# Kernel optimization log

Measured on AMD Instinct MI355X. Metric: run time of the kernel, lower is better.

Reference implementation:

```python
import jax, jax.numpy as jnp
import numpy as np
import math

HEADS = 16
LAYER, NUM_LAYERS = 6, 12
ALPHA = 1.0 - math.tanh(math.pi * LAYER / NUM_LAYERS)
EPS = 1e-5


def _rot_half(t):
    d = t.shape[-1] // 2
    return jnp.concatenate([-t[..., d:], t[..., :d]], axis=-1)


def axial_rope(t):
    # t: [b, n, H, W, d]. Axial rotary: height rotates first d/2, width rotates second d/2.
    H, W, d = t.shape[2], t.shape[3], t.shape[4]
    half = d // 2
    inv_freq = 1.0 / (10000.0 ** (jnp.arange(0, half, 2, dtype=jnp.float32) / half))  # [half/2]
    ang_h = jnp.arange(H, dtype=jnp.float32)[:, None] * inv_freq[None, :]  # [H, half/2]
    ang_w = jnp.arange(W, dtype=jnp.float32)[:, None] * inv_freq[None, :]  # [W, half/2]
    ang_h = jnp.concatenate([ang_h, ang_h], axis=-1)  # [H, half]
    ang_w = jnp.concatenate([ang_w, ang_w], axis=-1)  # [W, half]
    ch, sh = jnp.cos(ang_h)[:, None, :], jnp.sin(ang_h)[:, None, :]  # [H,1,half]
    cw, sw = jnp.cos(ang_w)[None, :, :], jnp.sin(ang_w)[None, :, :]  # [1,W,half]
    th, tw = t[..., :half], t[..., half:]
    th = th * ch + _rot_half(th) * sh
    tw = tw * cw + _rot_half(tw) * sw
    return jnp.concatenate([th, tw], axis=-1)


def setup_inputs() -> dict:
    key = jax.random.key(0)
    ks = jax.random.split(key, 4)
    b, H, W, hid = 32, 28, 28, 1024
    return {
        "x": jax.random.normal(ks[0], (b, H, W, hid), jnp.float32),
        "input_img": jax.random.normal(ks[1], (b, H, W, hid), jnp.float32),
        "qkv_w": jax.random.normal(ks[2], (hid, 3 * hid), jnp.float32) * 0.02,
        "o_w": jax.random.normal(ks[3], (hid, hid), jnp.float32) * 0.02,
        "gn_w": jnp.ones((HEADS,), jnp.float32),
        "gn_b": jnp.zeros((HEADS,), jnp.float32),
    }


def reference(x, input_img, qkv_w, o_w, gn_w, gn_b):
    b, H, W, hid = x.shape
    n, dh = HEADS, hid // HEADS
    qkv = x @ qkv_w  # [b,H,W,3*hid]
    # 'b h w (c d) -> c b h w d'
    qkv = qkv.reshape(b, H, W, 3, hid).transpose(3, 0, 1, 2, 4)
    qkv = qkv + input_img[None] * ALPHA
    # 'c b h w (n d) -> c b n h w d'; unpack order is q, v, k
    qkv = qkv.reshape(3, b, H, W, n, dh).transpose(0, 1, 4, 2, 3, 5)
    q, v, k = qkv[0], qkv[1], qkv[2]
    gamma = (1.0 - 2.0 ** (-5.0 - jnp.arange(n, dtype=jnp.float32)))[None, :, None, None, None]
    k = k * gamma
    q, k = axial_rope(q), axial_rope(k)
    # attention along the W axis per row: [b,n,H,W,W]
    scores = jnp.einsum('bnhxd,bnhzd->bnhxz', q, k)
    # original einsum sums v over heights h as well as over y
    vsum = v.sum(axis=2)  # [b,n,W,dh]
    out = jnp.einsum('bnxwy,bnyd->bnxwd', scores, vsum)  # [b,n,H,W,dh]
    # GroupNorm(num_heads, num_heads): normalize each head over (H,W,dh)
    mu = out.mean(axis=(2, 3, 4), keepdims=True)
    var = out.var(axis=(2, 3, 4), keepdims=True)
    out = (out - mu) / jnp.sqrt(var + EPS)
    out = out * gn_w[None, :, None, None, None] + gn_b[None, :, None, None, None]
    # 'b n h w d -> b h w (n d)'
    out = out.transpose(0, 2, 3, 1, 4).reshape(b, H, W, hid)
    return out @ o_w
```

## Files before the change

kernel.cpp:

```cpp
#include <hip/hip_runtime.h>
#include <cstdint>
#include <cstddef>

#define HEADS 16
#define DH 64
#define BH 28
#define BWW 28
#define BATCH 32
#define HID 1024
#define M_ROWS 25088
#define ALPHA_C 0.082847664332725576f
#define EPS_C 1e-5f

typedef unsigned short ushort_t;
typedef __attribute__((ext_vector_type(8))) short bf16x8;
typedef __attribute__((ext_vector_type(4))) float f32x4;

__device__ inline unsigned short f2bf(float f) {
  unsigned int u = __builtin_bit_cast(unsigned int, f);
  u = (u + 0x7fffu + ((u >> 16) & 1u)) >> 16;
  return (unsigned short)u;
}
__device__ inline float bf2f(unsigned short h) {
  unsigned int u = ((unsigned int)h) << 16;
  return __builtin_bit_cast(float, u);
}

__global__ __launch_bounds__(256) void detect_k(const ushort_t* __restrict__ x,
                                                const ushort_t* __restrict__ qw,
                                                int* __restrict__ flagp) {
  int tid = threadIdx.x;
  int big = 0;
  #pragma unroll
  for (int j = 0; j < 4; ++j) {
    float a = fabsf(bf2f(x[tid * 4 + j]));
    float b = fabsf(bf2f(qw[tid * 4 + j]));
    if (!(a < 1e3f)) big++;
    if (!(b < 1e3f)) big++;
  }
  __shared__ int cnt;
  if (tid == 0) cnt = 0;
  __syncthreads();
  if (big) atomicAdd(&cnt, big);
  __syncthreads();
  if (tid == 0) *flagp = (cnt == 0) ? 1 : 0;
}

__global__ __launch_bounds__(256) void prep_k(const void* __restrict__ x,
                                              const void* __restrict__ img,
                                              const int* __restrict__ flagp,
                                              unsigned* __restrict__ x_bf,
                                              unsigned* __restrict__ img_bf,
                                              unsigned* __restrict__ xsum,
                                              float2* __restrict__ imgsum) {
  const int blk = blockIdx.x;
  const int half = blk & 1;
  const int bw = blk >> 1;
  const int b = bw / BWW, w = bw % BWW;
  const int c = half * 512 + threadIdx.x * 2;
  const size_t base2 = (((size_t)(b * BH * BWW) + w) * HID + c) >> 1;
  const size_t hstr2 = (size_t)BWW * HID / 2;
  float sx0 = 0.f, sx1 = 0.f, si0 = 0.f, si1 = 0.f;
  if (*flagp) {
    const unsigned* xb = (const unsigned*)x;
    const unsigned* ib = (const unsigned*)img;
    for (int h = 0; h < BH; ++h) {
      unsigned ux = xb[base2 + h * hstr2];
      unsigned ui = ib[base2 + h * hstr2];
      sx0 += bf2f((ushort_t)(ux & 0xffffu)); sx1 += bf2f((ushort_t)(ux >> 16));
      si0 += bf2f((ushort_t)(ui & 0xffffu)); si1 += bf2f((ushort_t)(ui >> 16));
    }
  } else {
    const float2* xf = (const float2*)x;
    const float2* iff = (const float2*)img;
    for (int h = 0; h < BH; ++h) {
      float2 a = xf[base2 + h * hstr2];
      float2 g = iff[base2 + h * hstr2];
      x_bf[base2 + h * hstr2]   = ((unsigned)f2bf(a.y) << 16) | f2bf(a.x);
      img_bf[base2 + h * hstr2] = ((unsigned)f2bf(g.y) << 16) | f2bf(g.x);
      sx0 += a.x; sx1 += a.y;
      si0 += g.x; si1 += g.y;
    }
  }
  const size_t o2 = ((size_t)bw * HID + c) >> 1;
  xsum[o2] = ((unsigned)f2bf(sx1) << 16) | f2bf(sx0);
  imgsum[o2] = make_float2(si0 * ALPHA_C, si1 * ALPHA_C);
}

__global__ void transpose_any_k(const void* __restrict__ src, const int* __restrict__ flagp,
                                ushort_t* __restrict__ dst, int R, int C) {
  __shared__ float tile[32][33];
  int isbf = *flagp;
  int c0 = blockIdx.x * 32, r0 = blockIdx.y * 32;
  int tx = threadIdx.x, ty = threadIdx.y;
  const ushort_t* sb = (const ushort_t*)src;
  const float* sf = (const float*)src;
  #pragma unroll
  for (int i = ty; i < 32; i += 8) {
    size_t idx = (size_t)(r0 + i) * C + (c0 + tx);
    tile[i][tx] = isbf ? bf2f(sb[idx]) : sf[idx];
  }
  __syncthreads();
  #pragma unroll
  for (int i = ty; i < 32; i += 8)
    dst[(size_t)(c0 + i) * R + (r0 + tx)] = f2bf(tile[tx][i]);
}

#define BK 32

#define STAGE1(bufA, bufB, kk0) do {                                                             \
  const ushort_t* a0_ = aRow + (kk0);                                                            \
  const ushort_t* b0_ = bRow + (kk0);                                                            \
  __builtin_amdgcn_global_load_lds((const __attribute__((address_space(1))) unsigned int*)a0_,   \
      (__attribute__((address_space(3))) unsigned int*)((bufA) + tid * 8), 16, 0, 0);            \
  __builtin_amdgcn_global_load_lds((const __attribute__((address_space(1))) unsigned int*)(a0_ + (size_t)64 * K), \
      (__attribute__((address_space(3))) unsigned int*)((bufA) + 2048 + tid * 8), 16, 0, 0);     \
  __builtin_amdgcn_global_load_lds((const __attribute__((address_space(1))) unsigned int*)b0_,   \
      (__attribute__((address_space(3))) unsigned int*)((bufB) + tid * 8), 16, 0, 0);            \
  __builtin_amdgcn_global_load_lds((const __attribute__((address_space(1))) unsigned int*)(b0_ + (size_t)64 * K), \
      (__attribute__((address_space(3))) unsigned int*)((bufB) + 2048 + tid * 8), 16, 0, 0);     \
} while (0)

__global__ __launch_bounds__(256) void gemm_qkv_k(const void* __restrict__ x_raw,
                                                  const ushort_t* __restrict__ x_bf,
                                                  const ushort_t* __restrict__ Bt,
                                                  const void* __restrict__ img_raw,
                                                  const ushort_t* __restrict__ img_bf,
                                                  const int* __restrict__ flagp,
                                                  ushort_t* __restrict__ qbuf,
                                                  ushort_t* __restrict__ kbuf) {
  __shared__ ushort_t As[128 * BK];
  __shared__ ushort_t Bs[128 * BK];
  const int tid = threadIdx.x;
  const int K = 1024;
  const int ntile = 16;
  const int nt = blockIdx.x % ntile;
  const int n0 = (nt < 8) ? nt * 128 : nt * 128 + 1024;
  const int m0 = (blockIdx.x / ntile) * 128;
  const int lane = tid & 63;
  const int wave = tid >> 6;
  const int wm = (wave >> 1) * 64;
  const int wn = (wave & 1) * 64;
  const int fr = lane & 15;
  const int fq = lane >> 4;
  const int isbf = *flagp;
  const ushort_t* A  = isbf ? (const ushort_t*)x_raw   : x_bf;
  const ushort_t* IM = isbf ? (const ushort_t*)img_raw : img_bf;

  f32x4 acc[4][4] = {};
  const int srow = tid >> 2;
  const int skk  = (tid & 3) * 8;
  const ushort_t* aRow = A  + (size_t)(m0 + srow) * K + skk;
  const ushort_t* bRow = Bt + (size_t)(n0 + srow) * K + skk;

  for (int k0 = 0; k0 < K; k0 += BK) {
    __syncthreads();
    STAGE1(As, Bs, k0);
    __syncthreads();
    bf16x8 af[4], bfv[4];
    #pragma unroll
    for (int i = 0; i < 4; ++i)
      af[i] = *reinterpret_cast<const bf16x8*>(&As[(wm + i * 16 + fr) * BK + fq * 8]);
    #pragma unroll
    for (int i = 0; i < 4; ++i)
      bfv[i] = *reinterpret_cast<const bf16x8*>(&Bs[(wn + i * 16 + fr) * BK + fq * 8]);
    #pragma unroll
    for (int mi = 0; mi < 4; ++mi)
      #pragma unroll
      for (int ni = 0; ni < 4; ++ni)
        acc[mi][ni] = __builtin_amdgcn_mfma_f32_16x16x32_bf16(af[mi], bfv[ni], acc[mi][ni], 0, 0, 0);
  }

  const int colg = n0 + wn;
  const int t = colg >> 10;
  const int n = (colg & 1023) >> 6;
  const float gamma = 1.0f - exp2f(-5.0f - (float)n);
  const float invf = powf(10000.0f, -(float)fr / 16.0f);

  #pragma unroll
  for (int mi = 0; mi < 4; ++mi) {
    #pragma unroll
    for (int r = 0; r < 4; ++r) {
      int m = m0 + wm + mi * 16 + fq * 4 + r;
      int b = m / 784, rem = m % 784;
      int h = rem / 28, w = rem % 28;
      size_t ibase = (size_t)m * HID + n * DH + fr;
      float v0 = acc[mi][0][r] + bf2f(IM[ibase])      * ALPHA_C;
      float v1 = acc[mi][1][r] + bf2f(IM[ibase + 16]) * ALPHA_C;
      float v2 = acc[mi][2][r] + bf2f(IM[ibase + 32]) * ALPHA_C;
      float v3 = acc[mi][3][r] + bf2f(IM[ibase + 48]) * ALPHA_C;
      if (t == 2) { v0 *= gamma; v1 *= gamma; v2 *= gamma; v3 *= gamma; }
      float snh, csh, snw, csw;
      __sincosf((float)h * invf, &snh, &csh);
      __sincosf((float)w * invf, &snw, &csw);
      float o0 = v0 * csh - v1 * snh;
      float o1 = v1 * csh + v0 * snh;
      float o2 = v2 * csw - v3 * snw;
      float o3 = v3 * csw + v2 * snw;
      ushort_t* dst = (t == 0 ? qbuf : kbuf) +
          (((((size_t)b * HEADS + n) * BH + h) * BWW + w) * DH) + fr;
      dst[0]  = f2bf(o0);
      dst[16] = f2bf(o1);
      dst[32] = f2bf(o2);
      dst[48] = f2bf(o3);
    }
  }
}

__global__ __launch_bounds__(256) void vsum_gemm_k(const ushort_t* __restrict__ A,
                                                   const ushort_t* __restrict__ Bt,
                                                   const float* __restrict__ imgsum,
                                                   float* __restrict__ vsum) {
  __shared__ ushort_t As[128 * BK];
  __shared__ ushort_t Bs[128 * BK];
  const int tid = threadIdx.x;
  const int K = 1024;
  const int n0 = (blockIdx.x % 8) * 128;
  const int m0 = (blockIdx.x / 8) * 128;
  const int lane = tid & 63;
  const int wave = tid >> 6;
  const int wm = (wave >> 1) * 64;
  const int wn = (wave & 1) * 64;
  const int fr = lane & 15;
  const int fq = lane >> 4;

  f32x4 acc[4][4] = {};
  const int srow = tid >> 2;
  const int skk  = (tid & 3) * 8;
  const ushort_t* aRow = A  + (size_t)(m0 + srow) * K + skk;
  const ushort_t* bRow = Bt + (size_t)(n0 + srow) * K + skk;

  for (int k0 = 0; k0 < K; k0 += BK) {
    __syncthreads();
    STAGE1(As, Bs, k0);
    __syncthreads();
    bf16x8 af[4], bfv[4];
    #pragma unroll
    for (int i = 0; i < 4; ++i)
      af[i] = *reinterpret_cast<const bf16x8*>(&As[(wm + i * 16 + fr) * BK + fq * 8]);
    #pragma unroll
    for (int i = 0; i < 4; ++i)
      bfv[i] = *reinterpret_cast<const bf16x8*>(&Bs[(wn + i * 16 + fr) * BK + fq * 8]);
    #pragma unroll
    for (int mi = 0; mi < 4; ++mi)
      #pragma unroll
      for (int ni = 0; ni < 4; ++ni)
        acc[mi][ni] = __builtin_amdgcn_mfma_f32_16x16x32_bf16(af[mi], bfv[ni], acc[mi][ni], 0, 0, 0);
  }

  #pragma unroll
  for (int mi = 0; mi < 4; ++mi)
    #pragma unroll
    for (int r = 0; r < 4; ++r) {
      int m = m0 + wm + mi * 16 + fq * 4 + r;
      int b = m / BWW, w = m % BWW;
      #pragma unroll
      for (int ni = 0; ni < 4; ++ni) {
        int col = n0 + wn + ni * 16 + fr;
        int n = col >> 6, d = col & 63;
        vsum[((((size_t)b * HEADS + n) * BWW) + w) * DH + d] =
            acc[mi][ni][r] + imgsum[(size_t)m * HID + col];
      }
    }
}

__global__ __launch_bounds__(512) void attn_k(const ushort_t* __restrict__ qbuf,
                                              const ushort_t* __restrict__ kbuf,
                                              const float* __restrict__ vsum,
                                              const void* __restrict__ gn_w,
                                              const void* __restrict__ gn_b,
                                              const int* __restrict__ flagp,
                                              ushort_t* __restrict__ xo) {
  __shared__ __align__(16) ushort_t outL[BH * BWW * DH];
  __shared__ ushort_t Vt[64 * 32];
  __shared__ ushort_t Sa[8][32 * 32];
  __shared__ float rs[8][2];
  __shared__ float mu_s, rstd_s;
  const int bn = blockIdx.x;
  const int b = bn >> 4, n = bn & 15;
  const int tid = threadIdx.x;
  const int lane = tid & 63, wv = tid >> 6;
  const int fr = lane & 15, fq = lane >> 4;
  const size_t vbase = (size_t)bn * BWW * DH;

  for (int e = tid; e < 64 * 32; e += 512) {
    int d = e >> 5, y = e & 31;
    Vt[e] = (y < BWW) ? f2bf(vsum[vbase + (size_t)y * DH + d]) : (ushort_t)0;
  }
  __syncthreads();

  bf16x8 bv[4];
  #pragma unroll
  for (int i = 0; i < 4; ++i)
    bv[i] = *reinterpret_cast<const bf16x8*>(&Vt[(i * 16 + fr) * 32 + fq * 8]);

  float lsum = 0.f, lsq = 0.f;
  ushort_t* sa = Sa[wv];

  for (int hi = 0; hi < 4; ++hi) {
    const int h = wv + hi * 8;
    const bool act = (h < BH);
    const size_t qb = ((size_t)bn * BH + (act ? h : 0)) * BWW * DH;

    if (act) {
      f32x4 s[2][2] = {};
      #pragma unroll
      for (int kk = 0; kk < 2; ++kk) {
        bf16x8 qf[2], kf[2];
        #pragma unroll
        for (int t = 0; t < 2; ++t) {
          qf[t] = *reinterpret_cast<const bf16x8*>(qbuf + qb + (size_t)(t * 16 + fr) * DH + kk * 32 + fq * 8);
          kf[t] = *reinterpret_cast<const bf16x8*>(kbuf + qb + (size_t)(t * 16 + fr) * DH + kk * 32 + fq * 8);
        }
        #pragma unroll
        for (int mt = 0; mt < 2; ++mt)
          #pragma unroll
          for (int nt = 0; nt < 2; ++nt)
            s[mt][nt] = __builtin_amdgcn_mfma_f32_16x16x32_bf16(qf[mt], kf[nt], s[mt][nt], 0, 0, 0);
      }

      #pragma unroll
      for (int mt = 0; mt < 2; ++mt)
        #pragma unroll
        for (int nt = 0; nt < 2; ++nt)
          #pragma unroll
          for (int r = 0; r < 4; ++r)
            sa[(mt * 16 + fq * 4 + r) * 32 + nt * 16 + fr] = f2bf(s[mt][nt][r]);
    }
    __syncthreads();

    if (act) {
      f32x4 o[2][4] = {};
      #pragma unroll
      for (int mt = 0; mt < 2; ++mt) {
        bf16x8 af = *reinterpret_cast<const bf16x8*>(&sa[(mt * 16 + fr) * 32 + fq * 8]);
        #pragma unroll
        for (int nt = 0; nt < 4; ++nt)
          o[mt][nt] = __builtin_amdgcn_mfma_f32_16x16x32_bf16(af, bv[nt], o[mt][nt], 0, 0, 0);
      }

      #pragma unroll
      for (int mt = 0; mt < 2; ++mt)
        #pragma unroll
        for (int r = 0; r < 4; ++r) {
          int w_ = mt * 16 + fq * 4 + r;
          if (w_ < BWW) {
            ushort_t* dl = outL + ((size_t)(h * BWW + w_) * DH) + fr;
            #pragma unroll
            for (int nt = 0; nt < 4; ++nt) {
              float v = o[mt][nt][r];
              dl[nt * 16] = f2bf(v);
              lsum += v; lsq += v * v;
            }
          }
        }
    }
  }

  #pragma unroll
  for (int off = 32; off > 0; off >>= 1) {
    lsum += __shfl_down(lsum, off);
    lsq  += __shfl_down(lsq, off);
  }
  if (lane == 0) { rs[wv][0] = lsum; rs[wv][1] = lsq; }
  __syncthreads();
  if (tid == 0) {
    float s = 0.f, q2 = 0.f;
    #pragma unroll
    for (int i = 0; i < 8; ++i) { s += rs[i][0]; q2 += rs[i][1]; }
    const float Ninv = 1.0f / (float)(BH * BWW * DH);
    float mu = s * Ninv;
    float var = q2 * Ninv - mu * mu;
    mu_s = mu;
    rstd_s = rsqrtf(var + EPS_C);
  }
  __syncthreads();

  const int isbf = *flagp;
  const float gw = isbf ? bf2f(((const ushort_t*)gn_w)[n]) : ((const float*)gn_w)[n];
  const float gb = isbf ? bf2f(((const ushort_t*)gn_b)[n]) : ((const float*)gn_b)[n];
  const float sc = rstd_s * gw;
  const float sh_ = gb - mu_s * sc;
  for (int c = tid; c < BH * BWW * 8; c += 512) {
    int d8 = c & 7;
    int hw = c >> 3;
    int w = hw % BWW, h = hw / BWW;
    bf16x8 vv = *reinterpret_cast<const bf16x8*>(outL + (size_t)hw * DH + d8 * 8);
    union { ushort_t u[8]; uint4 q4; } o;
    #pragma unroll
    for (int j = 0; j < 8; ++j)
      o.u[j] = f2bf(bf2f((ushort_t)vv[j]) * sc + sh_);
    *(uint4*)(xo + (((size_t)(b * BH + h) * BWW + w) * HID) + n * DH + d8 * 8) = o.q4;
  }
}

__global__ __launch_bounds__(256) void gemm_bt_k(const ushort_t* __restrict__ A,
                                                 const ushort_t* __restrict__ Bt,
                                                 void* __restrict__ Cv,
                                                 const int* __restrict__ flagp,
                                                 int M, int N, int K) {
  __shared__ ushort_t As[128 * BK];
  __shared__ ushort_t Bs[128 * BK];
  const int tid = threadIdx.x;
  const int ntile = N / 128;
  const int n0 = (blockIdx.x % ntile) * 128;
  const int m0 = (blockIdx.x / ntile) * 128;
  const int lane = tid & 63;
  const int wave = tid >> 6;
  const int wm = (wave >> 1) * 64;
  const int wn = (wave & 1) * 64;
  const int fr = lane & 15;
  const int fq = lane >> 4;

  f32x4 acc[4][4] = {};
  const int srow = tid >> 2;
  const int skk  = (tid & 3) * 8;
  const ushort_t* aRow = A  + (size_t)(m0 + srow) * K + skk;
  const ushort_t* bRow = Bt + (size_t)(n0 + srow) * K + skk;

  for (int k0 = 0; k0 < K; k0 += BK) {
    __syncthreads();
    STAGE1(As, Bs, k0);
    __syncthreads();
    bf16x8 af[4], bfv[4];
    #pragma unroll
    for (int i = 0; i < 4; ++i)
      af[i] = *reinterpret_cast<const bf16x8*>(&As[(wm + i * 16 + fr) * BK + fq * 8]);
    #pragma unroll
    for (int i = 0; i < 4; ++i)
      bfv[i] = *reinterpret_cast<const bf16x8*>(&Bs[(wn + i * 16 + fr) * BK + fq * 8]);
    #pragma unroll
    for (int mi = 0; mi < 4; ++mi)
      #pragma unroll
      for (int ni = 0; ni < 4; ++ni)
        acc[mi][ni] = __builtin_amdgcn_mfma_f32_16x16x32_bf16(af[mi], bfv[ni], acc[mi][ni], 0, 0, 0);
  }

  int isbf = *flagp;
  if (isbf) {
    ushort_t* C = (ushort_t*)Cv;
    #pragma unroll
    for (int mi = 0; mi < 4; ++mi)
      #pragma unroll
      for (int r = 0; r < 4; ++r) {
        int m = m0 + wm + mi * 16 + fq * 4 + r;
        ushort_t* crow = C + (size_t)m * N + n0 + wn + fr;
        #pragma unroll
        for (int ni = 0; ni < 4; ++ni) crow[ni * 16] = f2bf(acc[mi][ni][r]);
      }
  } else {
    float* C = (float*)Cv;
    #pragma unroll
    for (int mi = 0; mi < 4; ++mi)
      #pragma unroll
      for (int r = 0; r < 4; ++r) {
        int m = m0 + wm + mi * 16 + fq * 4 + r;
        float* crow = C + (size_t)m * N + n0 + wn + fr;
        #pragma unroll
        for (int ni = 0; ni < 4; ++ni) crow[ni * 16] = acc[mi][ni][r];
      }
  }
}

extern "C" void kernel_launch(void* const* d_in, const int* in_sizes, int n_in,
                              void* d_out, int out_size, void* d_ws, size_t ws_size,
                              hipStream_t stream) {
  const void* x     = d_in[0];
  const void* img   = d_in[1];
  const void* qkv_w = d_in[2];
  const void* o_w   = d_in[3];
  const void* gn_w  = d_in[4];
  const void* gn_b  = d_in[5];

  char* ws = (char*)d_ws;
  ushort_t* x_bf   = (ushort_t*)(ws);
  ushort_t* xo     = (ushort_t*)(ws);
  ushort_t* qbuf   = (ushort_t*)(ws + 51380224);
  ushort_t* xsum   = (ushort_t*)(ws + 51380224);
  float*    imgsum = (float*)(ws + 53215232);
  ushort_t* kbuf   = (ushort_t*)(ws + 102760448);
  float*    vsum   = (float*)(ws + 154140672);
  int*      flag   = (int*)(ws + 157810688);
  ushort_t* w1T    = (ushort_t*)(ws + 157810944);
  ushort_t* w2T    = (ushort_t*)(ws + 164102400);
  ushort_t* img_bf = (ushort_t*)(ws + 166199552);

  detect_k<<<1, 256, 0, stream>>>((const ushort_t*)x, (const ushort_t*)qkv_w, flag);
  prep_k<<<BATCH * BWW * 2, 256, 0, stream>>>(x, img, flag,
      (unsigned*)x_bf, (unsigned*)img_bf, (unsigned*)xsum, (float2*)imgsum);
  transpose_any_k<<<dim3(96, 32), dim3(32, 8), 0, stream>>>(qkv_w, flag, w1T, 1024, 3072);
  transpose_any_k<<<dim3(32, 32), dim3(32, 8), 0, stream>>>(o_w, flag, w2T, 1024, 1024);

  vsum_gemm_k<<<56, 256, 0, stream>>>(xsum, w1T + (size_t)1024 * 1024, imgsum, vsum);
  gemm_qkv_k<<<196 * 16, 256, 0, stream>>>(x, x_bf, w1T, img, img_bf, flag, qbuf, kbuf);

  attn_k<<<BATCH * HEADS, 512, 0, stream>>>(qbuf, kbuf, vsum, gn_w, gn_b, flag, xo);
  gemm_bt_k<<<196 * 8, 256, 0, stream>>>(xo, w2T, d_out, flag, M_ROWS, 1024, 1024);
}
```

Baseline: 590.0 us.

## Rewrite QKV GEMM with 256x256 tiles, double-buffered LDS and swizzled layout

The QKV projection GEMM moves from 128x128 tiles with BK=32 and a single LDS buffer to 256x256 tiles with BK=64, 512 threads and two LDS buffers. Global-to-LDS loads for the next K step are interleaved with the MFMA phases of the current one, and an XOR swizzle is applied to avoid LDS bank conflicts. Wave priority is raised around the MFMA blocks. This aims to hide load latency and raise data reuse, at the cost of much more LDS and more registers, which may limit occupancy.

```diff
diff --git a/kernel.cpp b/kernel.cpp
--- a/kernel.cpp
+++ b/kernel.cpp
@@ -121,67 +121,149 @@
       (__attribute__((address_space(3))) unsigned int*)((bufB) + 2048 + tid * 8), 16, 0, 0);     \
 } while (0)
 
-__global__ __launch_bounds__(256) void gemm_qkv_k(const void* __restrict__ x_raw,
-                                                  const ushort_t* __restrict__ x_bf,
-                                                  const ushort_t* __restrict__ Bt,
-                                                  const void* __restrict__ img_raw,
-                                                  const ushort_t* __restrict__ img_bf,
-                                                  const int* __restrict__ flagp,
-                                                  ushort_t* __restrict__ qbuf,
-                                                  ushort_t* __restrict__ kbuf) {
-  __shared__ ushort_t As[128 * BK];
-  __shared__ ushort_t Bs[128 * BK];
+#define GLQ(ld, gs) __builtin_amdgcn_global_load_lds( \
+    (const __attribute__((address_space(1))) unsigned int*)(gs), \
+    (__attribute__((address_space(3))) unsigned int*)(ld), 16, 0, 0)
+#define RBAR() __builtin_amdgcn_s_barrier()
+#define LK0()  do { asm volatile("s_waitcnt lgkmcnt(0)" ::: "memory"); \
+                    __builtin_amdgcn_sched_barrier(0); } while (0)
+#define VM0()  do { asm volatile("s_waitcnt vmcnt(0)" ::: "memory"); \
+                    __builtin_amdgcn_sched_barrier(0); } while (0)
+
+__global__ __launch_bounds__(512, 2) void gemm_qkv_k(const void* __restrict__ x_raw,
+                                                     const ushort_t* __restrict__ x_bf,
+                                                     const ushort_t* __restrict__ Bt,
+                                                     const void* __restrict__ img_raw,
+                                                     const ushort_t* __restrict__ img_bf,
+                                                     const int* __restrict__ flagp,
+                                                     ushort_t* __restrict__ qbuf,
+                                                     ushort_t* __restrict__ kbuf) {
+  __shared__ ushort_t As2[2][256 * 64];
+  __shared__ ushort_t Bs2[2][256 * 64];
   const int tid = threadIdx.x;
-  const int K = 1024;
-  const int ntile = 16;
-  const int nt = blockIdx.x % ntile;
-  const int n0 = (nt < 8) ? nt * 128 : nt * 128 + 1024;
-  const int m0 = (blockIdx.x / ntile) * 128;
-  const int lane = tid & 63;
-  const int wave = tid >> 6;
-  const int wm = (wave >> 1) * 64;
-  const int wn = (wave & 1) * 64;
-  const int fr = lane & 15;
-  const int fq = lane >> 4;
+  const int nt = blockIdx.x & 7;
+  const int n0 = (nt < 4) ? nt * 256 : nt * 256 + 1024;
+  const int m0 = (blockIdx.x >> 3) * 256;
+  const int lane = tid & 63, wv = tid >> 6;
+  const int fr = lane & 15, fq = lane >> 4;
+  const int wr = wv >> 2, wc = wv & 3;
   const int isbf = *flagp;
   const ushort_t* A  = isbf ? (const ushort_t*)x_raw   : x_bf;
   const ushort_t* IM = isbf ? (const ushort_t*)img_raw : img_bf;
 
-  f32x4 acc[4][4] = {};
-  const int srow = tid >> 2;
-  const int skk  = (tid & 3) * 8;
-  const ushort_t* aRow = A  + (size_t)(m0 + srow) * K + skk;
-  const ushort_t* bRow = Bt + (size_t)(n0 + srow) * K + skk;
-
-  for (int k0 = 0; k0 < K; k0 += BK) {
-    __syncthreads();
-    STAGE1(As, Bs, k0);
-    __syncthreads();
-    bf16x8 af[4], bfv[4];
-    #pragma unroll
-    for (int i = 0; i < 4; ++i)
-      af[i] = *reinterpret_cast<const bf16x8*>(&As[(wm + i * 16 + fr) * BK + fq * 8]);
-    #pragma unroll
-    for (int i = 0; i < 4; ++i)
-      bfv[i] = *reinterpret_cast<const bf16x8*>(&Bs[(wn + i * 16 + fr) * BK + fq * 8]);
-    #pragma unroll
-    for (int mi = 0; mi < 4; ++mi)
-      #pragma unroll
-      for (int ni = 0; ni < 4; ++ni)
-        acc[mi][ni] = __builtin_amdgcn_mfma_f32_16x16x32_bf16(af[mi], bfv[ni], acc[mi][ni], 0, 0, 0);
-  }
-
-  const int colg = n0 + wn;
+  const int srow = tid >> 3;
+  const int scol = ((tid & 7) * 8) ^ ((srow & 7) << 3);
+  const ushort_t* aG = A  + (size_t)(m0 + srow) * 1024 + scol;
+  const ushort_t* bG = Bt + (size_t)(n0 + srow) * 1024 + scol;
+  const int dOff = tid * 8;
+
+  const int xr  = (fr & 7) << 3;
+  const int cx0 = (fq * 8) ^ xr;
+  const int cx1 = (32 + fq * 8) ^ xr;
+  const int aBase = (wr * 128 + fr) * 64;
+  const int bBase = (wc * 64 + fr) * 64;
+
+  f32x4 acc[8][4] = {};
+
+  {
+    ushort_t* dA = As2[0]; ushort_t* dB = Bs2[0];
+    #pragma unroll
+    for (int j = 0; j < 4; ++j) GLQ(dA + j * 4096 + dOff, aG + (size_t)j * 65536);
+    #pragma unroll
+    for (int j = 0; j < 4; ++j) GLQ(dB + j * 4096 + dOff, bG + (size_t)j * 65536);
+  }
+  VM0();
+  __syncthreads();
+
+  #pragma unroll 2
+  for (int kt = 0; kt < 16; ++kt) {
+    const ushort_t* sA = As2[kt & 1];
+    const ushort_t* sB = Bs2[kt & 1];
+    ushort_t* dA = As2[(kt + 1) & 1];
+    ushort_t* dB = Bs2[(kt + 1) & 1];
+    const int ke = (kt + 1) * 64;
+    const bool pf = kt < 15;
+    bf16x8 af[4], bf0[4], bf1[4];
+
+    #pragma unroll
+    for (int i = 0; i < 4; ++i) af[i]  = *(const bf16x8*)&sA[aBase + i * 1024 + cx0];
+    #pragma unroll
+    for (int i = 0; i < 4; ++i) bf0[i] = *(const bf16x8*)&sB[bBase + i * 1024 + cx0];
+    if (pf) {
+      GLQ(dA + dOff,            aG + ke);
+      GLQ(dA +  4096 + dOff,    aG +  65536 + ke);
+      GLQ(dA +  8192 + dOff,    aG + 131072 + ke);
+    }
+    RBAR(); LK0();
+    __builtin_amdgcn_s_setprio(1);
+    #pragma unroll
+    for (int i = 0; i < 4; ++i)
+      #pragma unroll
+      for (int j = 0; j < 4; ++j)
+        acc[i][j] = __builtin_amdgcn_mfma_f32_16x16x32_bf16(af[i], bf0[j], acc[i][j], 0, 0, 0);
+    __builtin_amdgcn_s_setprio(0);
+    RBAR();
+
+    #pragma unroll
+    for (int i = 0; i < 4; ++i) af[i] = *(const bf16x8*)&sA[aBase + (i + 4) * 1024 + cx0];
+    if (pf) {
+      GLQ(dA + 12288 + dOff,    aG + 196608 + ke);
+      GLQ(dB + dOff,            bG + ke);
+      GLQ(dB +  4096 + dOff,    bG +  65536 + ke);
+    }
+    RBAR(); LK0();
+    __builtin_amdgcn_s_setprio(1);
+    #pragma unroll
+    for (int i = 0; i < 4; ++i)
+      #pragma unroll
+      for (int j = 0; j < 4; ++j)
+        acc[i + 4][j] = __builtin_amdgcn_mfma_f32_16x16x32_bf16(af[i], bf0[j], acc[i + 4][j], 0, 0, 0);
+    __builtin_amdgcn_s_setprio(0);
+    RBAR();
+
+    #pragma unroll
+    for (int i = 0; i < 4; ++i) af[i]  = *(const bf16x8*)&sA[aBase + i * 1024 + cx1];
+    #pragma unroll
+    for (int i = 0; i < 4; ++i) bf1[i] = *(const bf16x8*)&sB[bBase + i * 1024 + cx1];
+    if (pf) {
+      GLQ(dB +  8192 + dOff,    bG + 131072 + ke);
+      GLQ(dB + 12288 + dOff,    bG + 196608 + ke);
+    }
+    RBAR(); LK0();
+    __builtin_amdgcn_s_setprio(1);
+    #pragma unroll
+    for (int i = 0; i < 4; ++i)
+      #pragma unroll
+      for (int j = 0; j < 4; ++j)
+        acc[i][j] = __builtin_amdgcn_mfma_f32_16x16x32_bf16(af[i], bf1[j], acc[i][j], 0, 0, 0);
+    __builtin_amdgcn_s_setprio(0);
+    RBAR();
+
+    #pragma unroll
+    for (int i = 0; i < 4; ++i) af[i] = *(const bf16x8*)&sA[aBase + (i + 4) * 1024 + cx1];
+    RBAR(); LK0();
+    __builtin_amdgcn_s_setprio(1);
+    #pragma unroll
+    for (int i = 0; i < 4; ++i)
+      #pragma unroll
+      for (int j = 0; j < 4; ++j)
+        acc[i + 4][j] = __builtin_amdgcn_mfma_f32_16x16x32_bf16(af[i], bf1[j], acc[i + 4][j], 0, 0, 0);
+    __builtin_amdgcn_s_setprio(0);
+    if (pf) VM0();
+    RBAR();
+  }
+
+  const int colg = n0 + wc * 64;
   const int t = colg >> 10;
   const int n = (colg & 1023) >> 6;
   const float gamma = 1.0f - exp2f(-5.0f - (float)n);
   const float invf = powf(10000.0f, -(float)fr / 16.0f);
 
   #pragma unroll
-  for (int mi = 0; mi < 4; ++mi) {
+  for (int mi = 0; mi < 8; ++mi) {
     #pragma unroll
     for (int r = 0; r < 4; ++r) {
-      int m = m0 + wm + mi * 16 + fq * 4 + r;
+      int m = m0 + wr * 128 + mi * 16 + fq * 4 + r;
       int b = m / 784, rem = m % 784;
       int h = rem / 28, w = rem % 28;
       size_t ibase = (size_t)m * HID + n * DH + fr;
@@ -492,7 +574,7 @@
   transpose_any_k<<<dim3(32, 32), dim3(32, 8), 0, stream>>>(o_w, flag, w2T, 1024, 1024);
 
   vsum_gemm_k<<<56, 256, 0, stream>>>(xsum, w1T + (size_t)1024 * 1024, imgsum, vsum);
-  gemm_qkv_k<<<196 * 16, 256, 0, stream>>>(x, x_bf, w1T, img, img_bf, flag, qbuf, kbuf);
+  gemm_qkv_k<<<98 * 8, 512, 0, stream>>>(x, x_bf, w1T, img, img_bf, flag, qbuf, kbuf);
 
   attn_k<<<BATCH * HEADS, 512, 0, stream>>>(qbuf, kbuf, vsum, gn_w, gn_b, flag, xo);
   gemm_bt_k<<<196 * 8, 256, 0, stream>>>(xo, w2T, d_out, flag, M_ROWS, 1024, 1024);
```

Measured after the change: 599.6 us. About the same (+1.6%).
